# Optimization experiments

Measured on AMD Instinct MI355X. Metric: run time of the kernel, lower is better.

The kernel has to match this reference:

```python
import jax, jax.numpy as jnp
import numpy as np

H, W = 80, 80
LOWPASS = 0.3   # 3DGS low-pass filter added to 2D covariance diagonal
NEAR = 0.2      # near-plane cull depth


def quat_to_rot(q):
    # q: [N,4] (w,x,y,z) -> [N,3,3]
    w, x, y, z = q[..., 0], q[..., 1], q[..., 2], q[..., 3]
    return jnp.stack([
        jnp.stack([1 - 2 * (y * y + z * z), 2 * (x * y - w * z), 2 * (x * z + w * y)], -1),
        jnp.stack([2 * (x * y + w * z), 1 - 2 * (x * x + z * z), 2 * (y * z - w * x)], -1),
        jnp.stack([2 * (x * z - w * y), 2 * (y * z + w * x), 1 - 2 * (x * x + y * y)], -1),
    ], -2)


def setup_inputs() -> dict:
    key = jax.random.key(0)
    k1, k2 = jax.random.split(key)
    vsize = 1.25
    def mids(lo, hi, lim):
        g = np.arange(lo, hi + 1e-6, vsize)
        return ((g[:-1] + g[1:]) / 2.0)[:lim]
    xy = mids(-20.0, 20.0, 200)   # 32 midpoints
    zz = mids(-4.0, 4.0, 16)      # 6 midpoints
    X, Y, Z = np.meshgrid(xy, xy, zz, indexing='ij')
    pc_xyz = jnp.asarray(np.stack([X, Y, Z], -1).reshape(-1, 3), jnp.float32)  # [6144,3]
    N = pc_xyz.shape[0]
    B, NC, C = 1, 6, 32
    vox_features = jax.random.normal(k1, (B, N, C), jnp.float32)
    density = jax.random.normal(k2, (B, N), jnp.float32)
    scales = jnp.full((N, 1), float(np.log(vsize)), jnp.float32)
    rots = jnp.concatenate([jnp.ones((N, 1)), jnp.zeros((N, 3))], -1).astype(jnp.float32)
    # 6 surround cameras at origin, yaw = k*60deg; cam axes: x=right, y=up-ish, z=forward
    yaws = np.arange(NC) * (2 * np.pi / NC)
    f = np.stack([np.cos(yaws), np.sin(yaws), np.zeros(NC)], -1)
    r = np.stack([np.sin(yaws), -np.cos(yaws), np.zeros(NC)], -1)
    u = np.cross(f, r)
    Rw2c = np.stack([r, u, f], 1)  # rows are camera axes -> world2cam rotation [NC,3,3]
    cam_rot = jnp.asarray(Rw2c[None], jnp.float32)          # [B,NC,3,3]
    cam_trans = jnp.zeros((B, NC, 3), jnp.float32)          # [B,NC,3]
    cam_intr = jnp.asarray(np.tile(np.array([45.0, 45.0, W / 2.0, H / 2.0], np.float32), (B, NC, 1)))
    return dict(vox_features=vox_features, density=density, cam_rot=cam_rot,
                cam_trans=cam_trans, cam_intr=cam_intr, pc_xyz=pc_xyz,
                scales=scales, rots=rots)


def _render_one(Rcw, t, intr, pc_xyz, Mcov, opacity, feats):
    # Rcw [3,3], t [3], intr [4]; Mcov [N,3,3] = R*diag(s); opacity [N]; feats [N,C]
    fx, fy, cx, cy = intr[0], intr[1], intr[2], intr[3]
    cam = pc_xyz @ Rcw.T + t                    # [N,3] camera-frame means
    tz = jnp.maximum(cam[:, 2], 1e-6)
    valid = (cam[:, 2] > NEAR).astype(pc_xyz.dtype)
    u = fx * cam[:, 0] / tz + cx
    v = fy * cam[:, 1] / tz + cy
    z0 = jnp.zeros_like(tz)
    J = jnp.stack([jnp.stack([fx / tz, z0, -fx * cam[:, 0] / tz ** 2], -1),
                   jnp.stack([z0, fy / tz, -fy * cam[:, 1] / tz ** 2], -1)], -2)  # [N,2,3]
    A = jnp.einsum('nij,jk->nik', J, Rcw)       # J @ W  [N,2,3]
    Bm = jnp.einsum('nij,njk->nik', A, Mcov)    # [N,2,3]
    cov = jnp.einsum('nij,nkj->nik', Bm, Bm)    # 2D covariance [N,2,2]
    a = cov[:, 0, 0] + LOWPASS
    b = cov[:, 0, 1]
    c = cov[:, 1, 1] + LOWPASS
    det = a * c - b * b
    ia, ib, ic = c / det, -b / det, a / det
    # depth-sort (invalid gaussians pushed to the back)
    order = jnp.argsort(tz + (1.0 - valid) * 1e6)
    u, v, ia, ib, ic = u[order], v[order], ia[order], ib[order], ic[order]
    op_s, feat_s, valid_s = opacity[order], feats[order], valid[order]
    px = jnp.arange(W, dtype=pc_xyz.dtype)
    py = jnp.arange(H, dtype=pc_xyz.dtype)
    dx = px[None, None, :] - u[:, None, None]   # [N,1,W] -> broadcast [N,H,W]
    dy = py[None, :, None] - v[:, None, None]   # [N,H,1]
    power = (-0.5 * (ia[:, None, None] * dx * dx + ic[:, None, None] * dy * dy)
             - ib[:, None, None] * dx * dy)
    g = jnp.exp(jnp.minimum(power, 0.0))
    alpha = jnp.clip(op_s[:, None, None] * g, 0.0, 0.99) * valid_s[:, None, None]
    Tcum = jnp.cumprod(1.0 - alpha, axis=0)
    Texc = jnp.concatenate([jnp.ones((1, H, W), alpha.dtype), Tcum[:-1]], 0)  # exclusive transmittance
    return jnp.einsum('nhw,nc->chw', Texc * alpha, feat_s)


def reference(vox_features, density, cam_rot, cam_trans, cam_intr, pc_xyz, scales, rots):
    Bsz, N, C = vox_features.shape
    Rg = quat_to_rot(rots)                      # [N,3,3]
    s = jnp.exp(scales)                         # [N,1] isotropic scale
    Mcov = Rg * s[:, :, None]                   # R @ diag(s,s,s)
    outs = []
    for b in range(Bsz):
        op = jax.nn.softplus(density[b]).reshape(-1)        # opacity activation
        feats = vox_features[b].reshape(-1, C)
        def rone(args):
            R_, t_, K_ = args
            return _render_one(R_, t_, K_, pc_xyz, Mcov, op, feats)
        out_b = jax.lax.map(rone, (cam_rot[b], cam_trans[b], cam_intr[b]))  # [NC,C,H,W]
        outs.append(out_b)
    return jnp.stack(outs)                      # [B,NC,C,H,W]
```

## Files before the change

kernel.cpp:

```cpp
#include <hip/hip_runtime.h>

#define NEARV    0.2f
#define LOWPASSV 0.3f

constexpr int HH = 80, WW = 80;
constexpr int CFE = 32;
constexpr int NZ = 6;

constexpr int STHREADS = 1024;
constexpr int SWAVES = 16;
constexpr int SBINS = 512;
constexpr int NCELL = 1024;
constexpr int HMAX = NCELL * NZ;

typedef unsigned long long u64;
typedef unsigned int u32;

__global__ __launch_bounds__(1024) void sort_kernel(
    const float* __restrict__ pc_xyz, const float* __restrict__ cam_rot,
    const float* __restrict__ cam_trans, int N,
    int* __restrict__ counts, int* __restrict__ cellord)
{
  __shared__ u32 skey[NCELL];
  __shared__ u32 spay[NCELL];
  __shared__ u32 whist[SWAVES * SBINS];
  __shared__ u32 binstart[SBINS];
  __shared__ u32 wpart[8];
  __shared__ int scount;

  const int cam = blockIdx.x;
  const int tid = threadIdx.x;
  const int wv = tid >> 6, ln = tid & 63;
  const float* R = cam_rot + cam*9;
  const float R20 = R[6], R21 = R[7], R22 = R[8];
  const float t2  = cam_trans[cam*3+2];
  if (tid == 0) scount = 0;
  __syncthreads();

  const int i0 = tid * NZ;
  u32 kk = 0x07FFFFFFu;
  bool valid = false;
  if (i0 < N) {
    float c2 = R20*pc_xyz[i0*3+0] + R21*pc_xyz[i0*3+1] + R22*pc_xyz[i0*3+2] + t2;
    if (c2 > NEARV) {
      u32 b = __float_as_uint(c2) - 0x3E000000u;
      kk = b < 0x07FFFFFEu ? b : 0x07FFFFFEu;
      valid = true;
    }
  }
  skey[tid] = kk; spay[tid] = (u32)tid;
  u64 vb = __ballot(valid);
  if (ln == 0) atomicAdd(&scount, __popcll(vb));

  for (int pass = 0; pass < 3; ++pass) {
    const int sh = pass * 9;
    for (int i = tid; i < SWAVES*SBINS; i += STHREADS) whist[i] = 0;
    __syncthreads();

    const u32 k = skey[tid];
    const u32 p = spay[tid];
    const int d = (int)((k >> sh) & 511u);
    u64 m = ~0ull;
    #pragma unroll
    for (int b = 0; b < 9; ++b) {
      u64 bb = __ballot((d >> b) & 1);
      m &= ((d >> b) & 1) ? bb : ~bb;
    }
    const u32 lower = (u32)__popcll(m & ((1ull << ln) - 1ull));
    if (lower == 0) whist[(wv << 9) + d] = (u32)__popcll(m);
    __syncthreads();

    if (tid < SBINS) {
      u32 t[SWAVES];
      #pragma unroll
      for (int w = 0; w < SWAVES; ++w) t[w] = whist[(w << 9) + tid];
      u32 tot = 0;
      #pragma unroll
      for (int w = 0; w < SWAVES; ++w) { u32 x = t[w]; whist[(w << 9) + tid] = tot; tot += x; }
      binstart[tid] = tot;
    }
    __syncthreads();
    u32 v = 0, inc = 0;
    if (tid < SBINS) {
      v = binstart[tid]; inc = v;
      #pragma unroll
      for (int off = 1; off < 64; off <<= 1) {
        u32 t = __shfl_up(inc, off);
        if (ln >= off) inc += t;
      }
      if (ln == 63) wpart[tid >> 6] = inc;
    }
    __syncthreads();
    if (tid < SBINS) {
      u32 add = 0;
      for (int i = 0; i < (tid >> 6); ++i) add += wpart[i];
      binstart[tid] = add + inc - v;
    }
    __syncthreads();

    const u32 pos = binstart[d] + whist[(wv << 9) + d] + lower;
    skey[pos] = k; spay[pos] = p;
    __syncthreads();
  }

  const int vc = scount;
  if (tid < vc) cellord[(size_t)cam * NCELL + tid] = (int)spay[tid];
  if (tid == 0) counts[cam] = vc * NZ;
}

__global__ __launch_bounds__(256) void proj_kernel(
    const float* __restrict__ pc_xyz, const float* __restrict__ cam_rot,
    const float* __restrict__ cam_trans, const float* __restrict__ cam_intr,
    const float* __restrict__ density, const float* __restrict__ scales,
    int N, int NC,
    const int* __restrict__ counts, const int* __restrict__ cellord,
    float4* __restrict__ hdrA, float4* __restrict__ hdrB)
{
  const int cam = blockIdx.y;
  const int kq = blockIdx.x * 256 + threadIdx.x;
  if (kq >= counts[cam]) return;

  const int cellp = kq / NZ;
  const int n = cellord[(size_t)cam * NCELL + cellp] * NZ + (kq - cellp * NZ);

  const float* R = cam_rot + cam*9;
  const float* t = cam_trans + cam*3;
  const float* intr = cam_intr + cam*4;
  const float fx = intr[0], fy = intr[1], cx = intr[2], cy = intr[3];
  const int b = cam / NC;

  const float p0 = pc_xyz[n*3+0], p1 = pc_xyz[n*3+1], p2 = pc_xyz[n*3+2];
  const float c0 = R[0]*p0 + R[1]*p1 + R[2]*p2 + t[0];
  const float c1 = R[3]*p0 + R[4]*p1 + R[5]*p2 + t[1];
  const float c2 = R[6]*p0 + R[7]*p1 + R[8]*p2 + t[2];
  const float tz = fmaxf(c2, 1e-6f);
  const float itz = 1.0f / tz;
  const float u = fx*c0*itz + cx;
  const float v = fy*c1*itz + cy;
  const float j00 = fx*itz, j02 = -(fx*c0*itz)*itz;
  const float j11 = fy*itz, j12 = -(fy*c1*itz)*itz;
  const float s = expf(scales[n]);
  const float s2 = s*s;
  const float cov00 = s2*(j00*j00 + j02*j02);
  const float cov01 = s2*(j02*j12);
  const float cov11 = s2*(j11*j11 + j12*j12);
  const float a = cov00 + LOWPASSV, bb = cov01, cc = cov11 + LOWPASSV;
  const float det = a*cc - bb*bb;
  const float idet = 1.0f / det;
  const float mid = 0.5f*(a + cc);
  const float dd = sqrtf(fmaxf(mid*mid - det, 0.f));
  float r2 = 32.f * (mid + dd);
  const float dens = density[(size_t)b*N + n];
  const float op = fmaxf(dens, 0.f) + log1pf(expf(-fabsf(dens)));
  const float sx = fminf(fmaxf(u, 0.f), (float)(WW-1)) - u;
  const float sy = fminf(fmaxf(v, 0.f), (float)(HH-1)) - v;
  if (sx*sx + sy*sy > r2) r2 = -1.0f;

  hdrA[(size_t)cam * HMAX + kq] = make_float4(u, v, cc*idet, -bb*idet);
  hdrB[(size_t)cam * HMAX + kq] = make_float4(a*idet, op, r2, __int_as_float(n));
}

__global__ __launch_bounds__(64) void render_kernel(
    const float* __restrict__ vox,
    const float4* __restrict__ hdrA, const float4* __restrict__ hdrB,
    const int* __restrict__ counts,
    float* __restrict__ out, int N, int NC)
{
  __shared__ float4 cA[64], cB[64];
  __shared__ int   cgi[64];
  __shared__ float4 sfeat[64];

  const int cam = blockIdx.y;
  const int tile = blockIdx.x;
  const int tx = tile % (WW/8), ty = tile / (WW/8);
  const int lane = threadIdx.x;
  const int p  = lane & 31;
  const int h  = lane >> 5;
  const int lx = p & 7, ly = p >> 3;
  const int px = tx*8 + lx, py = ty*4 + ly;
  const float fpx = (float)px, fpy = (float)py;
  const float tx0 = (float)(tx*8), tx1 = tx0 + 7.f;
  const float ty0 = (float)(ty*4), ty1 = ty0 + 3.f;
  const int count = counts[cam];
  const int b = cam / NC;
  const float4* hA = hdrA + (size_t)cam * HMAX;
  const float4* hB = hdrB + (size_t)cam * HMAX;
  const float4* voxb = (const float4*)vox + (size_t)b * N * (CFE/4);

  float acc[CFE/2];
  #pragma unroll
  for (int i = 0; i < CFE/2; ++i) acc[i] = 0.f;
  float T = 1.0f;
  bool done = false;

  if (count > 0) {
    const int kcf = min(lane, count - 1);
    float4 na = hA[kcf], nb = hB[kcf];

    for (int k0 = 0; k0 < count && !done; k0 += 64) {
      const float4 a0 = na, b0 = nb;
      if (k0 + 64 < count) {
        const int kn = min(k0 + 64 + lane, count - 1);
        na = hA[kn]; nb = hB[kn];
      }
      const int ki = k0 + lane;
      const float ddx = fminf(fmaxf(a0.x, tx0), tx1) - a0.x;
      const float ddy = fminf(fmaxf(a0.y, ty0), ty1) - a0.y;
      const bool hit = (ki < count) && (ddx*ddx + ddy*ddy <= b0.z);
      const u64 m = __ballot(hit);
      const int P = __popcll(m);
      if (P == 0) continue;
      __syncthreads();
      if (hit) {
        const int pos = (int)__popcll(m & ((1ull << lane) - 1ull));
        cA[pos] = a0;
        cB[pos] = b0;
        cgi[pos] = __float_as_int(b0.w);
      }
      __syncthreads();

      const int sl = lane >> 3, sc = lane & 7;
      float4 pf = voxb[(size_t)cgi[min(sl, P - 1)] * (CFE/4) + sc];

      for (int j = 0; j < P; j += 8) {
        sfeat[lane] = pf;
        if (j + 8 < P) {
          const int si = min(j + 8 + sl, P - 1);
          pf = voxb[(size_t)cgi[si] * (CFE/4) + sc];
        }
        __syncthreads();

        float al[8];
        #pragma unroll
        for (int qq = 0; qq < 8; ++qq) {
          const int idx = j + qq;
          const float4 a1 = cA[idx & 63];
          const float4 a2 = cB[idx & 63];
          const float dx = fpx - a1.x, dy = fpy - a1.y;
          const float power = -0.5f*(a1.z*dx*dx + a2.x*dy*dy) - a1.w*dx*dy;
          float av = fminf(a2.y * __expf(fminf(power, 0.f)), 0.99f);
          av = (power > -16.f) ? av : 0.f;
          al[qq] = (idx < P) ? av : 0.f;
        }
        #pragma unroll
        for (int qq = 0; qq < 8; ++qq) {
          const float w = T * al[qq];
          T -= w;
          if (__any(w > 1e-8f)) {
            const float4* fj = &sfeat[qq * 8 + 4 * h];
            #pragma unroll
            for (int c4 = 0; c4 < 4; ++c4) {
              const float4 fv = fj[c4];
              acc[c4*4+0] += w*fv.x; acc[c4*4+1] += w*fv.y;
              acc[c4*4+2] += w*fv.z; acc[c4*4+3] += w*fv.w;
            }
          }
        }
        if (__all(T < 1e-3f)) { done = true; break; }
        __syncthreads();
      }
    }
  }
  float* ob = out + (((size_t)cam * CFE + 16*h) * HH + py) * WW + px;
  #pragma unroll
  for (int c = 0; c < CFE/2; ++c) ob[(size_t)c * HH * WW] = acc[c];
}

extern "C" void kernel_launch(void* const* d_in, const int* in_sizes, int n_in,
                              void* d_out, int out_size, void* d_ws, size_t ws_size,
                              hipStream_t stream) {
  const float* vox       = (const float*)d_in[0];
  const float* density   = (const float*)d_in[1];
  const float* cam_rot   = (const float*)d_in[2];
  const float* cam_trans = (const float*)d_in[3];
  const float* cam_intr  = (const float*)d_in[4];
  const float* pc_xyz    = (const float*)d_in[5];
  const float* scales    = (const float*)d_in[6];
  float* out = (float*)d_out;

  const int N    = in_sizes[5] / 3;
  const int NCAM = in_sizes[4] / 4;
  const int B    = in_sizes[1] / N;
  const int NC   = NCAM / B;

  unsigned char* ws = (unsigned char*)d_ws;
  int* countsPtr = (int*)ws;
  int* cellord   = (int*)(ws + 256);
  float4* hdrA   = (float4*)(ws + 32768);
  float4* hdrB   = (float4*)(ws + 32768 + (size_t)NCAM * HMAX * sizeof(float4));

  sort_kernel<<<dim3(NCAM), STHREADS, 0, stream>>>(
      pc_xyz, cam_rot, cam_trans, N, countsPtr, cellord);
  proj_kernel<<<dim3((HMAX + 255) / 256, NCAM), 256, 0, stream>>>(
      pc_xyz, cam_rot, cam_trans, cam_intr, density, scales, N, NC,
      countsPtr, cellord, hdrA, hdrB);
  render_kernel<<<dim3((WW/8)*(HH/4), NCAM), 64, 0, stream>>>(
      vox, hdrA, hdrB, countsPtr, out, N, NC);
}
```

Before: 84.16 us.

## Replace 1024-thread radix sort with single-wave bitonic sort of packed keys

The per-camera depth sort drops its 1024-thread, three-pass radix sort with histograms and scans. In its place, one 64-lane wavefront runs a bitonic sort over 1024 packed keys, each holding a truncated 22-bit depth and a 10-bit cell index. The valid count now comes from a wave shuffle reduction instead of a shared atomic. This shrinks the launch footprint and the many block barriers, but runs all 55 bitonic stages serially in one wave and truncates depth precision, which could reorder near-equal depths.

```diff
diff --git a/kernel.cpp b/kernel.cpp
--- a/kernel.cpp
+++ b/kernel.cpp
@@ -7,105 +7,70 @@
 constexpr int CFE = 32;
 constexpr int NZ = 6;
 
-constexpr int STHREADS = 1024;
-constexpr int SWAVES = 16;
-constexpr int SBINS = 512;
 constexpr int NCELL = 1024;
 constexpr int HMAX = NCELL * NZ;
 
 typedef unsigned long long u64;
 typedef unsigned int u32;
 
-__global__ __launch_bounds__(1024) void sort_kernel(
+__global__ __launch_bounds__(64) void sort_kernel(
     const float* __restrict__ pc_xyz, const float* __restrict__ cam_rot,
     const float* __restrict__ cam_trans, int N,
     int* __restrict__ counts, int* __restrict__ cellord)
 {
-  __shared__ u32 skey[NCELL];
-  __shared__ u32 spay[NCELL];
-  __shared__ u32 whist[SWAVES * SBINS];
-  __shared__ u32 binstart[SBINS];
-  __shared__ u32 wpart[8];
-  __shared__ int scount;
+  __shared__ u32 sk[NCELL];
 
   const int cam = blockIdx.x;
-  const int tid = threadIdx.x;
-  const int wv = tid >> 6, ln = tid & 63;
+  const int lane = threadIdx.x;
   const float* R = cam_rot + cam*9;
   const float R20 = R[6], R21 = R[7], R22 = R[8];
   const float t2  = cam_trans[cam*3+2];
-  if (tid == 0) scount = 0;
+
+  int myvalid = 0;
+  #pragma unroll
+  for (int e = 0; e < NCELL/64; ++e) {
+    const int cell = e*64 + lane;
+    const int i0 = cell * NZ;
+    u32 key22 = 0x3FFFFFu;
+    if (i0 < N) {
+      float c2 = R20*pc_xyz[i0*3+0] + R21*pc_xyz[i0*3+1] + R22*pc_xyz[i0*3+2] + t2;
+      if (c2 > NEARV) {
+        u32 b = __float_as_uint(c2) - 0x3E000000u;
+        b = b < 0x03FFFF00u ? b : 0x03FFFF00u;
+        key22 = b >> 4;
+        ++myvalid;
+      }
+    }
+    sk[cell] = (key22 << 10) | (u32)cell;
+  }
   __syncthreads();
 
-  const int i0 = tid * NZ;
-  u32 kk = 0x07FFFFFFu;
-  bool valid = false;
-  if (i0 < N) {
-    float c2 = R20*pc_xyz[i0*3+0] + R21*pc_xyz[i0*3+1] + R22*pc_xyz[i0*3+2] + t2;
-    if (c2 > NEARV) {
-      u32 b = __float_as_uint(c2) - 0x3E000000u;
-      kk = b < 0x07FFFFFEu ? b : 0x07FFFFFEu;
-      valid = true;
+  for (int k = 2; k <= NCELL; k <<= 1) {
+    for (int j = k >> 1; j > 0; j >>= 1) {
+      #pragma unroll
+      for (int pp = 0; pp < NCELL/128; ++pp) {
+        const int p = pp*64 + lane;
+        const int i = ((p & ~(j-1)) << 1) | (p & (j-1));
+        const int q = i + j;
+        const bool up = ((i & k) == 0);
+        const u32 x = sk[i], y = sk[q];
+        const bool sw = up ? (x > y) : (x < y);
+        sk[i] = sw ? y : x;
+        sk[q] = sw ? x : y;
+      }
+      __syncthreads();
     }
   }
-  skey[tid] = kk; spay[tid] = (u32)tid;
-  u64 vb = __ballot(valid);
-  if (ln == 0) atomicAdd(&scount, __popcll(vb));
-
-  for (int pass = 0; pass < 3; ++pass) {
-    const int sh = pass * 9;
-    for (int i = tid; i < SWAVES*SBINS; i += STHREADS) whist[i] = 0;
-    __syncthreads();
-
-    const u32 k = skey[tid];
-    const u32 p = spay[tid];
-    const int d = (int)((k >> sh) & 511u);
-    u64 m = ~0ull;
-    #pragma unroll
-    for (int b = 0; b < 9; ++b) {
-      u64 bb = __ballot((d >> b) & 1);
-      m &= ((d >> b) & 1) ? bb : ~bb;
-    }
-    const u32 lower = (u32)__popcll(m & ((1ull << ln) - 1ull));
-    if (lower == 0) whist[(wv << 9) + d] = (u32)__popcll(m);
-    __syncthreads();
-
-    if (tid < SBINS) {
-      u32 t[SWAVES];
-      #pragma unroll
-      for (int w = 0; w < SWAVES; ++w) t[w] = whist[(w << 9) + tid];
-      u32 tot = 0;
-      #pragma unroll
-      for (int w = 0; w < SWAVES; ++w) { u32 x = t[w]; whist[(w << 9) + tid] = tot; tot += x; }
-      binstart[tid] = tot;
-    }
-    __syncthreads();
-    u32 v = 0, inc = 0;
-    if (tid < SBINS) {
-      v = binstart[tid]; inc = v;
-      #pragma unroll
-      for (int off = 1; off < 64; off <<= 1) {
-        u32 t = __shfl_up(inc, off);
-        if (ln >= off) inc += t;
-      }
-      if (ln == 63) wpart[tid >> 6] = inc;
-    }
-    __syncthreads();
-    if (tid < SBINS) {
-      u32 add = 0;
-      for (int i = 0; i < (tid >> 6); ++i) add += wpart[i];
-      binstart[tid] = add + inc - v;
-    }
-    __syncthreads();
-
-    const u32 pos = binstart[d] + whist[(wv << 9) + d] + lower;
-    skey[pos] = k; spay[pos] = p;
-    __syncthreads();
-  }
-
-  const int vc = scount;
-  if (tid < vc) cellord[(size_t)cam * NCELL + tid] = (int)spay[tid];
-  if (tid == 0) counts[cam] = vc * NZ;
+
+  #pragma unroll
+  for (int off = 32; off > 0; off >>= 1) myvalid += __shfl_down(myvalid, off, 64);
+
+  #pragma unroll
+  for (int e = 0; e < NCELL/64; ++e) {
+    const int r = e*64 + lane;
+    cellord[(size_t)cam * NCELL + r] = (int)(sk[r] & 1023u);
+  }
+  if (lane == 0) counts[cam] = myvalid * NZ;
 }
 
 __global__ __launch_bounds__(256) void proj_kernel(
@@ -289,7 +254,7 @@
   float4* hdrA   = (float4*)(ws + 32768);
   float4* hdrB   = (float4*)(ws + 32768 + (size_t)NCAM * HMAX * sizeof(float4));
 
-  sort_kernel<<<dim3(NCAM), STHREADS, 0, stream>>>(
+  sort_kernel<<<dim3(NCAM), 64, 0, stream>>>(
       pc_xyz, cam_rot, cam_trans, N, countsPtr, cellord);
   proj_kernel<<<dim3((HMAX + 255) / 256, NCAM), 256, 0, stream>>>(
       pc_xyz, cam_rot, cam_trans, cam_intr, density, scales, N, NC,
```

Result: slower. 116.8 us (+38.8%).
